# Performance work log

Hardware: AMD Instinct MI355X
Metric: run time of the kernel (lower is better)

The kernel has to match this reference:

```python
import jax, jax.numpy as jnp
import numpy as np

N = 100000
E = 1600000
R = 8
DIN = 128
H = 128
C = 16
NROOT = 1024


def rgcn_conv(x, src, dst, edge_type, w_rel, w_root, bias):
    """PyG RGCNConv: per-relation mean aggregation + root weight + bias."""
    n, din = x.shape
    r = w_rel.shape[0]
    msgs = x[src]  # [E, din] gather
    seg = dst * r + edge_type  # combined (node, relation) segment id
    sums = jax.ops.segment_sum(msgs, seg, num_segments=n * r)        # [N*R, din]
    cnt = jax.ops.segment_sum(jnp.ones((msgs.shape[0],), x.dtype), seg,
                              num_segments=n * r)                    # [N*R]
    mean = sums / jnp.maximum(cnt, 1.0)[:, None]
    mean = mean.reshape(n, r, din)
    # relation-specific transform then sum over relations, plus root transform
    out = jnp.einsum('nrd,rde->ne', mean, w_rel) + x @ w_root + bias
    return out


def setup_inputs() -> dict:
    key = jax.random.key(0)
    ks = jax.random.split(key, 16)
    s = 0.05
    return {
        'x': jax.random.normal(ks[0], (N, DIN), jnp.float32),
        'edge_index': jax.random.randint(ks[1], (2, E), 0, N, jnp.int64),
        'edge_type': jax.random.randint(ks[2], (E,), 0, R, jnp.int64),
        'root_idx': jax.random.randint(ks[3], (NROOT,), 0, N, jnp.int64),
        'wrel1': jax.random.normal(ks[4], (R, DIN, H), jnp.float32) * s,
        'root1': jax.random.normal(ks[5], (DIN, H), jnp.float32) * s,
        'b1': jax.random.normal(ks[6], (H,), jnp.float32) * s,
        'wrel2': jax.random.normal(ks[7], (R, H, H), jnp.float32) * s,
        'root2': jax.random.normal(ks[8], (H, H), jnp.float32) * s,
        'b2': jax.random.normal(ks[9], (H,), jnp.float32) * s,
        'wrel3': jax.random.normal(ks[10], (R, H, C), jnp.float32) * s,
        'root3': jax.random.normal(ks[11], (H, C), jnp.float32) * s,
        'b3': jax.random.normal(ks[12], (C,), jnp.float32) * s,
    }


def reference(x, edge_index, edge_type, root_idx,
              wrel1, root1, b1, wrel2, root2, b2, wrel3, root3, b3):
    src, dst = edge_index[0], edge_index[1]
    h = jax.nn.relu(rgcn_conv(x, src, dst, edge_type, wrel1, root1, b1))
    # hidden conv (relu; dropout is identity in eval mode)
    h = jax.nn.relu(rgcn_conv(h, src, dst, edge_type, wrel2, root2, b2))
    # final conv, no activation
    h = rgcn_conv(h, src, dst, edge_type, wrel3, root3, b3)
    return h[root_idx]  # [NROOT, C]
```

## Files before the change

### kernel.cpp

```cpp
#include <hip/hip_runtime.h>
#include <hip/hip_fp16.h>


typedef _Float16 f16;
typedef _Float16 f16x2 __attribute__((ext_vector_type(2)));
typedef _Float16 f16x4 __attribute__((ext_vector_type(4)));
typedef _Float16 f16x8 __attribute__((ext_vector_type(8)));
typedef float f32x4 __attribute__((ext_vector_type(4)));

#define NREL 8
#define ACHUNK 8192

__global__ void k_hist(const int* __restrict__ dst, int E, int* __restrict__ cnt) {
  int e = blockIdx.x * 256 + threadIdx.x;
  if (e < E) atomicAdd(&cnt[dst[e]], 1);
}

__global__ void k_scan1(const int* __restrict__ in, int* __restrict__ out,
                        int* __restrict__ part, int n) {
  __shared__ int sh[256];
  int b = blockIdx.x, t = threadIdx.x;
  int base = b * 4096 + t * 16;
  int v[16]; int s = 0;
#pragma unroll
  for (int j = 0; j < 16; j++) { int idx = base + j; int x = (idx < n) ? in[idx] : 0; v[j] = s; s += x; }
  sh[t] = s; __syncthreads();
  for (int off = 1; off < 256; off <<= 1) {
    int x = 0; if (t >= off) x = sh[t - off];
    __syncthreads();
    if (t >= off) sh[t] += x;
    __syncthreads();
  }
  int excl = (t == 0) ? 0 : sh[t - 1];
  if (t == 255) part[b] = sh[255];
#pragma unroll
  for (int j = 0; j < 16; j++) { int idx = base + j; if (idx < n) out[idx] = v[j] + excl; }
}

__global__ void k_scan2(int* __restrict__ part, int nb) {
  __shared__ int sh[256];
  int t = threadIdx.x;
  sh[t] = (t < nb) ? part[t] : 0; __syncthreads();
  for (int off = 1; off < 256; off <<= 1) {
    int x = 0; if (t >= off) x = sh[t - off];
    __syncthreads();
    if (t >= off) sh[t] += x;
    __syncthreads();
  }
  if (t < nb) part[t] = (t == 0) ? 0 : sh[t - 1];
}

__global__ void k_scan3(int* __restrict__ out, const int* __restrict__ part, int n) {
  int i = blockIdx.x * 256 + threadIdx.x;
  if (i < n) out[i] += part[i >> 12];
}

__global__ void k_scatter(const int* __restrict__ src, const int* __restrict__ dstv,
                          const int* __restrict__ et, int E,
                          const int* __restrict__ off, int* __restrict__ fill,
                          int* __restrict__ sps) {
  int e = blockIdx.x * 256 + threadIdx.x;
  if (e >= E) return;
  int d = dstv[e];
  int pos = off[d] + atomicAdd(&fill[d], 1);
  sps[pos] = src[e] | (et[e] << 20);
}

__global__ void k_sentinel(int* __restrict__ p, int v) { *p = v; }

__global__ __launch_bounds__(256) void k_bhist(const int* __restrict__ dstv, int E,
                                               int* __restrict__ bcnt, int nbuck) {
  __shared__ int h[512];
  int t = threadIdx.x;
  for (int i = t; i < 512; i += 256) h[i] = 0;
  __syncthreads();
  int lo = blockIdx.x * ACHUNK;
  int hi = lo + ACHUNK < E ? lo + ACHUNK : E;
  for (int e = lo + t; e < hi; e += 256) atomicAdd(&h[dstv[e] >> 8], 1);
  __syncthreads();
  for (int i = t; i < nbuck; i += 256)
    if (h[i]) atomicAdd(&bcnt[i], h[i]);
}

__global__ __launch_bounds__(512) void k_bscan(const int* __restrict__ bcnt,
                                               int* __restrict__ boff, int nbuck) {
  __shared__ int sh[512];
  int t = threadIdx.x;
  sh[t] = (t < nbuck) ? bcnt[t] : 0;
  __syncthreads();
  for (int o = 1; o < 512; o <<= 1) {
    int v = 0; if (t >= o) v = sh[t - o];
    __syncthreads();
    sh[t] += v;
    __syncthreads();
  }
  if (t <= nbuck && t < 512) boff[t] = (t == 0) ? 0 : sh[t - 1];
  if (t == 511 && nbuck >= 512) boff[nbuck] = sh[511];
}

__global__ __launch_bounds__(256) void k_bucketA(
    const int* __restrict__ src, const int* __restrict__ dstv,
    const int* __restrict__ et, int E, const int* __restrict__ boff,
    int* __restrict__ bfill, int* __restrict__ tmp, int nbuck) {
  __shared__ int hist[512];
  __shared__ int base[512];
  int t = threadIdx.x;
  int lo = blockIdx.x * ACHUNK;
  int hi = lo + ACHUNK < E ? lo + ACHUNK : E;
  for (int i = t; i < nbuck; i += 256) hist[i] = 0;
  __syncthreads();
  for (int e = lo + t; e < hi; e += 256)
    atomicAdd(&hist[dstv[e] >> 8], 1);
  __syncthreads();
  for (int i = t; i < nbuck; i += 256) {
    int c = hist[i];
    base[i] = c ? (boff[i] + atomicAdd(&bfill[i], c)) : 0;
  }
  __syncthreads();
  for (int e = lo + t; e < hi; e += 256) {
    int d = dstv[e];
    int b = d >> 8;
    int pos = atomicAdd(&base[b], 1);
    tmp[pos] = src[e] | (et[e] << 20) | ((d & 255) << 23);
  }
}

__global__ __launch_bounds__(256) void k_bucketB2(const int* __restrict__ tmp,
                                                  const int* __restrict__ boff,
                                                  int* __restrict__ off,
                                                  int* __restrict__ sps, int N) {
  __shared__ int cnt[256];
  __shared__ int sh[256];
  __shared__ int loff[257];
  int b = blockIdx.x, t = threadIdx.x;
  int n0 = b << 8;
  int nn = (N - n0) < 256 ? (N - n0) : 256;
  cnt[t] = 0;
  __syncthreads();
  int e0 = boff[b], e1 = boff[b + 1];
  for (int e = e0 + t; e < e1; e += 256)
    atomicAdd(&cnt[(tmp[e] >> 23) & 255], 1);
  __syncthreads();
  sh[t] = cnt[t];
  __syncthreads();
  for (int o = 1; o < 256; o <<= 1) {
    int v = 0; if (t >= o) v = sh[t - o];
    __syncthreads();
    sh[t] += v;
    __syncthreads();
  }
  loff[t] = (t == 0) ? 0 : sh[t - 1];
  if (t == 255) loff[256] = sh[255];
  __syncthreads();
  if (t < nn) off[n0 + t] = e0 + loff[t];
  cnt[t] = 0;
  __syncthreads();
  for (int e = e0 + t; e < e1; e += 256) {
    int v = tmp[e];
    int dl = (v >> 23) & 255;
    int pos = e0 + loff[dl] + atomicAdd(&cnt[dl], 1);
    sps[pos] = v & 0x7FFFFF;
  }
}

__global__ void k_mark(const int* __restrict__ ridx, const int* __restrict__ off,
                       const int* __restrict__ sps, int* __restrict__ mark) {
  int i = blockIdx.x, t = threadIdx.x;
  int n = ridx[i];
  if (t == 0) mark[n] = 1;
  int e0 = off[n], e1 = off[n + 1];
  for (int e = e0 + t; e < e1; e += 64) mark[sps[e] & 0xFFFFF] = 1;
}

__global__ __launch_bounds__(256) void k_sinvp(const int* __restrict__ sps,
                                               const int* __restrict__ off,
                                               float* __restrict__ sinvp, int N) {
  __shared__ int c[16][8];
  int t = threadIdx.x;
  int g = t >> 4, st = t & 15;
  int n = blockIdx.x * 16 + g;
  if (st < 8) c[g][st] = 0;
  __syncthreads();
  if (n < N) {
    int e0 = off[n], e1 = off[n + 1];
    for (int e = e0 + st; e < e1; e += 16)
      atomicAdd(&c[g][((unsigned)sps[e]) >> 20], 1);
  }
  __syncthreads();
  if (n < N && st < 8) {
    int cc = c[g][st];
    sinvp[n * 8 + st] = 1.0f / (float)(cc > 1 ? cc : 1);
  }
}

__global__ void k_f32_to_f16(const float* __restrict__ in, f16* __restrict__ out, int n4) {
  int i = blockIdx.x * 256 + threadIdx.x;
  if (i < n4) {
    float4 v = ((const float4*)in)[i];
    f16x4 o; o[0] = (f16)v.x; o[1] = (f16)v.y; o[2] = (f16)v.z; o[3] = (f16)v.w;
    ((f16x4*)out)[i] = o;
  }
}

__global__ void k_tpw(const float* __restrict__ wrel, const float* __restrict__ wroot,
                      f16* __restrict__ dst, int PW, int p) {
  int row = blockIdx.x, k = threadIdx.x;
  float v = 0.f;
  if (row < 9 * PW) {
    int cb = row / PW, j = row - cb * PW;
    int col = p * PW + j;
    v = (cb < 8) ? wrel[(size_t)cb * 16384 + k * 128 + col] : wroot[k * 128 + col];
  }
  dst[(size_t)row * 128 + k] = (f16)v;
}

__global__ __launch_bounds__(256, 4) void k_gemm2(const f16* __restrict__ A,
                                                  const f16* __restrict__ Bt,
                                                  f16* __restrict__ C, int M, int ncol) {
  __shared__ f16 As[128 * 136];
  int tid = threadIdx.x;
  int m0 = blockIdx.y * 128, n0 = blockIdx.x * 128;
#pragma unroll
  for (int cch = 0; cch < 8; cch++) {
    int ci = tid + cch * 256;
    int row = ci >> 4, c8 = ci & 15;
    int gm = m0 + row;
    f16x8 va = {};
    if (gm < M) va = *(const f16x8*)(A + (size_t)gm * 128 + c8 * 8);
    *(f16x8*)(As + row * 136 + c8 * 8) = va;
  }
  __syncthreads();
  int wid = tid >> 6, lane = tid & 63;
  int wm = (wid & 1) * 64, wn = (wid >> 1) * 64;
  int lm = lane & 15, lk = lane >> 4;
  f32x4 acc[4][4] = {};
#pragma unroll
  for (int ks = 0; ks < 4; ks++) {
    int k0 = ks * 32;
    f16x8 a[4], b[4];
#pragma unroll
    for (int j = 0; j < 4; j++)
      b[j] = *(const f16x8*)(Bt + (size_t)(n0 + wn + j * 16 + lm) * 128 + k0 + lk * 8);
#pragma unroll
    for (int i = 0; i < 4; i++)
      a[i] = *(const f16x8*)(As + (wm + i * 16 + lm) * 136 + k0 + lk * 8);
#pragma unroll
    for (int i = 0; i < 4; i++)
#pragma unroll
      for (int j = 0; j < 4; j++)
        acc[i][j] = __builtin_amdgcn_mfma_f32_16x16x32_f16(a[i], b[j], acc[i][j], 0, 0, 0);
  }
  __syncthreads();
  f16* H = As;
#pragma unroll
  for (int i = 0; i < 4; i++)
#pragma unroll
    for (int j = 0; j < 4; j++)
#pragma unroll
      for (int q = 0; q < 4; q++)
        H[(wm + i * 16 + lk * 4 + q) * 136 + wn + j * 16 + lm] = (f16)acc[i][j][q];
  __syncthreads();
  for (int i = tid; i < 128 * 16; i += 256) {
    int row = i >> 4, c8 = i & 15;
    int gm = m0 + row, gn = n0 + c8 * 8;
    if (gm < M && gn < ncol)
      *(f16x8*)(C + (size_t)gm * ncol + gn) = *(const f16x8*)(H + row * 136 + c8 * 8);
  }
}

template <int PW>
__global__ __launch_bounds__(256) void k_edge_v(
    const f16* __restrict__ Y, const int* __restrict__ sps,
    const int* __restrict__ off, const float* __restrict__ sinvp,
    const float* __restrict__ bias, f16* __restrict__ hout,
    const int* __restrict__ mark, int N, int pass) {
  constexpr int CPL = PW / 16;
  constexpr int LDY = 9 * PW;
  int t = threadIdx.x;
  int g = t >> 4, st = t & 15;
  int n = blockIdx.x * 16 + g;
  if (n >= N) return;
  if (mark && !mark[n]) return;
  float sv = (st < 8) ? sinvp[n * 8 + st] : 0.f;
  int e0 = off[n], e1 = off[n + 1];
  float a[CPL], b2[CPL];
  {
    const f16* rp = Y + (size_t)n * LDY + 8 * PW + st * CPL;
    const float* bp = bias + pass * PW + st * CPL;
#pragma unroll
    for (int q = 0; q < CPL; q++) { a[q] = (float)rp[q] + bp[q]; b2[q] = 0.f; }
  }
  int sgbase = t & 48;
  int e = e0;
  for (; e + 1 < e1; e += 2) {
    int p0 = sps[e], p1 = sps[e + 1];
    int s0 = p0 & 0xFFFFF, ty0 = ((unsigned)p0) >> 20;
    int s1 = p1 & 0xFFFFF, ty1 = ((unsigned)p1) >> 20;
    float sc0 = __shfl(sv, sgbase | ty0);
    float sc1 = __shfl(sv, sgbase | ty1);
    const f16* q0 = Y + (size_t)s0 * LDY + ty0 * PW + st * CPL;
    const f16* q1 = Y + (size_t)s1 * LDY + ty1 * PW + st * CPL;
    if constexpr (PW == 64) {
      f16x4 v0 = *(const f16x4*)q0;
      f16x4 v1 = *(const f16x4*)q1;
      a[0] += (float)v0[0] * sc0; a[1] += (float)v0[1] * sc0;
      a[2] += (float)v0[2] * sc0; a[3] += (float)v0[3] * sc0;
      b2[0] += (float)v1[0] * sc1; b2[1] += (float)v1[1] * sc1;
      b2[2] += (float)v1[2] * sc1; b2[3] += (float)v1[3] * sc1;
    } else {
      f16x2 v0 = *(const f16x2*)q0;
      f16x2 v1 = *(const f16x2*)q1;
      a[0] += (float)v0[0] * sc0; a[1] += (float)v0[1] * sc0;
      b2[0] += (float)v1[0] * sc1; b2[1] += (float)v1[1] * sc1;
    }
  }
  if (e < e1) {
    int p0 = sps[e];
    int s0 = p0 & 0xFFFFF, ty0 = ((unsigned)p0) >> 20;
    float sc0 = __shfl(sv, sgbase | ty0);
    const f16* q0 = Y + (size_t)s0 * LDY + ty0 * PW + st * CPL;
    if constexpr (PW == 64) {
      f16x4 v0 = *(const f16x4*)q0;
      a[0] += (float)v0[0] * sc0; a[1] += (float)v0[1] * sc0;
      a[2] += (float)v0[2] * sc0; a[3] += (float)v0[3] * sc0;
    } else {
      f16x2 v0 = *(const f16x2*)q0;
      a[0] += (float)v0[0] * sc0; a[1] += (float)v0[1] * sc0;
    }
  }
  if constexpr (PW == 64) {
    f16x4 o;
#pragma unroll
    for (int q = 0; q < 4; q++) o[q] = (f16)fmaxf(a[q] + b2[q], 0.f);
    *(f16x4*)(hout + (size_t)n * 128 + pass * PW + st * 4) = o;
  } else {
    f16x2 o;
#pragma unroll
    for (int q = 0; q < 2; q++) o[q] = (f16)fmaxf(a[q] + b2[q], 0.f);
    *(f16x2*)(hout + (size_t)n * 128 + pass * PW + st * 2) = o;
  }
}

__global__ __launch_bounds__(128) void k_layer3(const f16* __restrict__ h2,
                                                const int* __restrict__ sps,
                                                const int* __restrict__ off,
                                                const float* __restrict__ sinvp,
                                                const int* __restrict__ ridx,
                                                const float* __restrict__ wrel,
                                                const float* __restrict__ wroot,
                                                const float* __restrict__ b3,
                                                float* __restrict__ out) {
  __shared__ f16 W[9 * 2048];
  __shared__ float red[2][16];
  __shared__ float sinv_s[8];
  int t = threadIdx.x;
  int n = ridx[blockIdx.x];
  for (int j = t; j < 9 * 2048; j += 128)
    W[j] = (f16)((j < 8 * 2048) ? wrel[j] : wroot[j - 8 * 2048]);
  if (t < 8) sinv_s[t] = sinvp[n * 8 + t];
  __syncthreads();
  int e0 = off[n], e1 = off[n + 1];
  int c = t & 15, kg = t >> 4;
  float a = 0.f;
  for (int e = e0; e < e1; e++) {
    int ps = sps[e];
    int s = ps & 0xFFFFF, ty = ((unsigned)ps) >> 20;
    float p = 0.f;
#pragma unroll
    for (int j = 0; j < 16; j++) {
      int k = kg * 16 + j;
      p += (float)h2[(size_t)s * 128 + k] * (float)W[ty * 2048 + k * 16 + c];
    }
    a += sinv_s[ty] * p;
  }
  {
    float p = 0.f;
#pragma unroll
    for (int j = 0; j < 16; j++) {
      int k = kg * 16 + j;
      p += (float)h2[(size_t)n * 128 + k] * (float)W[8 * 2048 + k * 16 + c];
    }
    a += p;
  }
  a += __shfl_xor(a, 16);
  a += __shfl_xor(a, 32);
  if ((t & 63) < 16) red[t >> 6][t & 15] = a;
  __syncthreads();
  if (t < 16) out[(size_t)blockIdx.x * 16 + t] = red[0][t] + red[1][t] + b3[t];
}

extern "C" void kernel_launch(void* const* d_in, const int* in_sizes, int n_in,
                              void* d_out, int out_size, void* d_ws, size_t ws_size,
                              hipStream_t stream) {
  const float* x     = (const float*)d_in[0];
  const int*   eidx  = (const int*)d_in[1];
  const int*   etyp  = (const int*)d_in[2];
  const int*   ridx  = (const int*)d_in[3];
  const float* wrel1 = (const float*)d_in[4];
  const float* root1 = (const float*)d_in[5];
  const float* b1    = (const float*)d_in[6];
  const float* wrel2 = (const float*)d_in[7];
  const float* root2 = (const float*)d_in[8];
  const float* b2    = (const float*)d_in[9];
  const float* wrel3 = (const float*)d_in[10];
  const float* root3 = (const float*)d_in[11];
  const float* b3    = (const float*)d_in[12];

  int N = in_sizes[0] / 128;
  int E = in_sizes[2];
  int NROOT = in_sizes[3];
  const int* esrc = eidx;
  const int* edst = eidx + E;

  char* p = (char*)d_ws;
  auto alloc = [&](size_t bytes) { void* r = (void*)p; p += (bytes + 255) & ~(size_t)255; return r; };
  int*   off   = (int*)alloc((size_t)(N + 1) * 4);
  int*   sps   = (int*)alloc((size_t)E * 4);
  f16*   h1    = (f16*)alloc((size_t)N * 128 * 2);
  f16*   h2    = (f16*)alloc((size_t)N * 128 * 2);
  int*   mark  = (int*)alloc((size_t)N * 4);
  float* sinvp = (float*)alloc((size_t)N * 8 * 4);
  f16*   Wt    = (f16*)alloc((size_t)640 * 128 * 2);
  int*   bcnt  = (int*)alloc(512 * 4);
  int*   boff  = (int*)alloc(513 * 4);
  int*   bfill = (int*)alloc(512 * 4);

  size_t used = (size_t)(p - (char*)d_ws);
  size_t remain = ws_size > used ? ws_size - used : 0;
  int PW = (remain >= (size_t)N * 9 * 64 * 2 + (1u << 20)) ? 64 : 32;
  int ldy = 9 * PW;
  f16* Y = (f16*)alloc((size_t)N * ldy * 2);
  int* tmp  = (int*)Y;
  int* part = tmp + E;
  int* fill = part + 4096;

  int nbuck = (N + 255) >> 8;
  int nbA = (E + ACHUNK - 1) / ACHUNK;
  hipMemsetAsync(mark, 0, (size_t)N * 4, stream);

  if (nbuck <= 512) {
    hipMemsetAsync(bcnt, 0, 512 * 4, stream);
    hipMemsetAsync(bfill, 0, 512 * 4, stream);
    k_bhist<<<nbA, 256, 0, stream>>>(edst, E, bcnt, nbuck);
    k_bscan<<<1, 512, 0, stream>>>(bcnt, boff, nbuck);
    k_bucketA<<<nbA, 256, 0, stream>>>(esrc, edst, etyp, E, boff, bfill, tmp, nbuck);
    k_bucketB2<<<nbuck, 256, 0, stream>>>(tmp, boff, off, sps, N);
    k_sentinel<<<1, 1, 0, stream>>>(off + N, E);
  } else {
    int eb = (E + 255) / 256;
    hipMemsetAsync(off, 0, (size_t)(N + 1) * 4, stream);
    hipMemsetAsync(fill, 0, (size_t)N * 4, stream);
    k_hist<<<eb, 256, 0, stream>>>(edst, E, off);
    int nb1 = (N + 4095) / 4096;
    k_scan1<<<nb1, 256, 0, stream>>>(off, off, part, N);
    k_scan2<<<1, 256, 0, stream>>>(part, nb1);
    k_scan3<<<(N + 255) / 256, 256, 0, stream>>>(off, part, N);
    k_sentinel<<<1, 1, 0, stream>>>(off + N, E);
    k_scatter<<<eb, 256, 0, stream>>>(esrc, edst, etyp, E, off, fill, sps);
  }
  k_mark<<<NROOT, 64, 0, stream>>>(ridx, off, sps, mark);
  int ng16 = (N + 15) / 16;
  k_sinvp<<<ng16, 256, 0, stream>>>(sps, off, sinvp, N);
  k_f32_to_f16<<<((N * 32) + 255) / 256, 256, 0, stream>>>(x, h2, N * 32);

  int mb = (N + 127) / 128;
  int NT = (ldy + 127) / 128;
  int npass = 128 / PW;

  for (int ps = 0; ps < npass; ps++) {
    k_tpw<<<NT * 128, 128, 0, stream>>>(wrel1, root1, Wt, PW, ps);
    k_gemm2<<<dim3(NT, mb), 256, 0, stream>>>(h2, Wt, Y, N, ldy);
    if (PW == 64)
      k_edge_v<64><<<ng16, 256, 0, stream>>>(Y, sps, off, sinvp, b1, h1, nullptr, N, ps);
    else
      k_edge_v<32><<<ng16, 256, 0, stream>>>(Y, sps, off, sinvp, b1, h1, nullptr, N, ps);
  }
  for (int ps = 0; ps < npass; ps++) {
    k_tpw<<<NT * 128, 128, 0, stream>>>(wrel2, root2, Wt, PW, ps);
    k_gemm2<<<dim3(NT, mb), 256, 0, stream>>>(h1, Wt, Y, N, ldy);
    if (PW == 64)
      k_edge_v<64><<<ng16, 256, 0, stream>>>(Y, sps, off, sinvp, b2, h2, mark, N, ps);
    else
      k_edge_v<32><<<ng16, 256, 0, stream>>>(Y, sps, off, sinvp, b2, h2, mark, N, ps);
  }
  k_layer3<<<NROOT, 128, 0, stream>>>(h2, sps, off, sinvp, ridx, wrel3, root3, b3,
                                      (float*)d_out);
}
```

Baseline: 487.8 us.

## Keep A tile in registers and loop over all N tiles per block

The GEMM now launches one block per 128-row M tile and loops over every 128-column N tile inside the block. The A fragments are loaded from LDS into registers once and reused across all N tiles, so A is no longer reloaded from global memory for each N tile. MFMA operands are swapped so the accumulator layout allows packed f16x4 stores into LDS before the coalesced global write. The cost is far fewer blocks, less parallelism and more register pressure, since the min-blocks launch bound is dropped.

New measurement: 494.4 us. About the same (+1.3%).

```diff
diff --git a/kernel.cpp b/kernel.cpp
--- a/kernel.cpp
+++ b/kernel.cpp
@@ -214,12 +214,12 @@
   dst[(size_t)row * 128 + k] = (f16)v;
 }
 
-__global__ __launch_bounds__(256, 4) void k_gemm2(const f16* __restrict__ A,
-                                                  const f16* __restrict__ Bt,
-                                                  f16* __restrict__ C, int M, int ncol) {
+__global__ __launch_bounds__(256) void k_gemm3(const f16* __restrict__ A,
+                                               const f16* __restrict__ Bt,
+                                               f16* __restrict__ C, int M, int ncol) {
   __shared__ f16 As[128 * 136];
   int tid = threadIdx.x;
-  int m0 = blockIdx.y * 128, n0 = blockIdx.x * 128;
+  int m0 = blockIdx.x * 128;
 #pragma unroll
   for (int cch = 0; cch < 8; cch++) {
     int ci = tid + cch * 256;
@@ -233,38 +233,47 @@
   int wid = tid >> 6, lane = tid & 63;
   int wm = (wid & 1) * 64, wn = (wid >> 1) * 64;
   int lm = lane & 15, lk = lane >> 4;
-  f32x4 acc[4][4] = {};
-#pragma unroll
-  for (int ks = 0; ks < 4; ks++) {
-    int k0 = ks * 32;
-    f16x8 a[4], b[4];
-#pragma unroll
-    for (int j = 0; j < 4; j++)
-      b[j] = *(const f16x8*)(Bt + (size_t)(n0 + wn + j * 16 + lm) * 128 + k0 + lk * 8);
+  f16x8 af[4][4];
+#pragma unroll
+  for (int ks = 0; ks < 4; ks++)
 #pragma unroll
     for (int i = 0; i < 4; i++)
-      a[i] = *(const f16x8*)(As + (wm + i * 16 + lm) * 136 + k0 + lk * 8);
+      af[ks][i] = *(const f16x8*)(As + (wm + i * 16 + lm) * 136 + ks * 32 + lk * 8);
+  __syncthreads();
+  f16* H = As;
+  int NT = (ncol + 127) >> 7;
+  for (int nt = 0; nt < NT; nt++) {
+    int n0 = nt * 128;
+    f32x4 acc[4][4] = {};
+#pragma unroll
+    for (int ks = 0; ks < 4; ks++) {
+      f16x8 b[4];
+#pragma unroll
+      for (int j = 0; j < 4; j++)
+        b[j] = *(const f16x8*)(Bt + (size_t)(n0 + wn + j * 16 + lm) * 128 + ks * 32 + lk * 8);
+#pragma unroll
+      for (int i = 0; i < 4; i++)
+#pragma unroll
+        for (int j = 0; j < 4; j++)
+          acc[i][j] = __builtin_amdgcn_mfma_f32_16x16x32_f16(b[j], af[ks][i], acc[i][j], 0, 0, 0);
+    }
 #pragma unroll
     for (int i = 0; i < 4; i++)
 #pragma unroll
-      for (int j = 0; j < 4; j++)
-        acc[i][j] = __builtin_amdgcn_mfma_f32_16x16x32_f16(a[i], b[j], acc[i][j], 0, 0, 0);
-  }
-  __syncthreads();
-  f16* H = As;
-#pragma unroll
-  for (int i = 0; i < 4; i++)
-#pragma unroll
-    for (int j = 0; j < 4; j++)
-#pragma unroll
-      for (int q = 0; q < 4; q++)
-        H[(wm + i * 16 + lk * 4 + q) * 136 + wn + j * 16 + lm] = (f16)acc[i][j][q];
-  __syncthreads();
-  for (int i = tid; i < 128 * 16; i += 256) {
-    int row = i >> 4, c8 = i & 15;
-    int gm = m0 + row, gn = n0 + c8 * 8;
-    if (gm < M && gn < ncol)
-      *(f16x8*)(C + (size_t)gm * ncol + gn) = *(const f16x8*)(H + row * 136 + c8 * 8);
+      for (int j = 0; j < 4; j++) {
+        f16x4 o;
+        o[0] = (f16)acc[i][j][0]; o[1] = (f16)acc[i][j][1];
+        o[2] = (f16)acc[i][j][2]; o[3] = (f16)acc[i][j][3];
+        *(f16x4*)(H + (wm + i * 16 + lm) * 136 + wn + j * 16 + lk * 4) = o;
+      }
+    __syncthreads();
+    for (int i = tid; i < 128 * 16; i += 256) {
+      int row = i >> 4, c8 = i & 15;
+      int gm = m0 + row, gn = n0 + c8 * 8;
+      if (gm < M && gn < ncol)
+        *(f16x8*)(C + (size_t)gm * ncol + gn) = *(const f16x8*)(H + row * 136 + c8 * 8);
+    }
+    __syncthreads();
   }
 }
 
@@ -469,7 +478,7 @@
 
   for (int ps = 0; ps < npass; ps++) {
     k_tpw<<<NT * 128, 128, 0, stream>>>(wrel1, root1, Wt, PW, ps);
-    k_gemm2<<<dim3(NT, mb), 256, 0, stream>>>(h2, Wt, Y, N, ldy);
+    k_gemm3<<<mb, 256, 0, stream>>>(h2, Wt, Y, N, ldy);
     if (PW == 64)
       k_edge_v<64><<<ng16, 256, 0, stream>>>(Y, sps, off, sinvp, b1, h1, nullptr, N, ps);
     else
@@ -477,7 +486,7 @@
   }
   for (int ps = 0; ps < npass; ps++) {
     k_tpw<<<NT * 128, 128, 0, stream>>>(wrel2, root2, Wt, PW, ps);
-    k_gemm2<<<dim3(NT, mb), 256, 0, stream>>>(h1, Wt, Y, N, ldy);
+    k_gemm3<<<mb, 256, 0, stream>>>(h1, Wt, Y, N, ldy);
     if (PW == 64)
       k_edge_v<64><<<ng16, 256, 0, stream>>>(Y, sps, off, sinvp, b2, h2, mark, N, ps);
     else
```
